# Performance work log

Hardware: AMD Instinct MI355X
Metric: run time of the kernel (lower is better)

Reference implementation:

```python
import jax, jax.numpy as jnp
import numpy as np
import math

L, B = 1024, 256
SEQ_DIM, KMER_DIM, HID = 16, 256, 64
N_LAYERS = 2
IN_DIM = SEQ_DIM + KMER_DIM + 21  # 293


def _normalize(v, eps=1e-12):
    return v / jnp.maximum(jnp.linalg.norm(v, axis=-1, keepdims=True), eps)


def _nerf_rot(a, b, c):
    # rotation matrix with columns [bc, n x bc, n] from last three backbone points
    bc = _normalize(c - b)
    n = _normalize(jnp.cross(b - a, bc))
    return jnp.stack([bc, jnp.cross(n, bc), n], axis=-1)  # (..., 3, 3)


def pnerf(c_tilde, nfrag):
    # c_tilde: (3L, B, 3) SRF coordinates; parallelized natural extension of reference frame
    Ltot, batch = c_tilde.shape[0], c_tilde.shape[1]
    k = Ltot // nfrag
    # contiguous fragments of length k, folded into the batch dim: (k, nfrag*B, 3)
    x = c_tilde.reshape(nfrag, k, batch, 3).transpose(1, 0, 2, 3).reshape(k, nfrag * batch, 3)
    init = jnp.array([[-math.sqrt(0.5), math.sqrt(1.5), 0.0],
                      [-math.sqrt(2.0), 0.0, 0.0],
                      [0.0, 0.0, 0.0]], dtype=c_tilde.dtype)
    F = nfrag * batch
    carry0 = (jnp.broadcast_to(init[0], (F, 3)),
              jnp.broadcast_to(init[1], (F, 3)),
              jnp.broadcast_to(init[2], (F, 3)))

    def extend(carry, ct):
        a, b, c = carry
        R = _nerf_rot(a, b, c)                      # (F, 3, 3)
        d = c + jnp.einsum('fij,fj->fi', R, ct)     # (F, 3)
        return (b, c, d), d

    _, frag = jax.lax.scan(extend, carry0, x)        # (k, F, 3)
    frag = frag.reshape(k, nfrag, batch, 3).transpose(1, 0, 2, 3)  # (nfrag, k, B, 3)

    # assemble fragments sequentially; init frame is identity/origin so frag 0 passes through
    carryA = (jnp.broadcast_to(init[0], (batch, 3)),
              jnp.broadcast_to(init[1], (batch, 3)),
              jnp.broadcast_to(init[2], (batch, 3)))

    def assemble(carry, fr):
        a, b, c = carry
        R = _nerf_rot(a, b, c)                      # (B, 3, 3)
        y = c + jnp.einsum('bij,kbj->kbi', R, fr)   # (k, B, 3)
        return (y[-3], y[-2], y[-1]), y

    _, ys = jax.lax.scan(assemble, carryA, frag)     # (nfrag, k, B, 3)
    return ys.reshape(nfrag * k, batch, 3)


def setup_inputs() -> dict:
    key = jax.random.key(0)
    ks = jax.random.split(key, 12)
    s = 0.05
    return {
        'seq': jax.random.randint(ks[0], (L, B), 0, 20, dtype=jnp.int64),
        'kmer': jax.random.randint(ks[1], (L, B), 0, 22 ** 3, dtype=jnp.int64),
        'pssm': jax.random.uniform(ks[2], (L, B, 21), dtype=jnp.float32),
        'length': jax.random.randint(ks[3], (L,), 1, L, dtype=jnp.int64),
        'seq_embed': jax.random.normal(ks[4], (20, SEQ_DIM), dtype=jnp.float32) * s,
        'kmer_embed': jax.random.normal(ks[5], (22 ** 3, KMER_DIM), dtype=jnp.float32) * s,
        'W0': jax.random.normal(ks[6], (IN_DIM, HID), dtype=jnp.float32) * s,
        'b0': jnp.zeros((HID,), dtype=jnp.float32),
        'We': jax.random.normal(ks[7], (HID, HID), dtype=jnp.float32) * s,
        'be': jnp.zeros((HID,), dtype=jnp.float32),
        'W1': jax.random.normal(ks[8], (HID, 9), dtype=jnp.float32) * s,
        'b1': jnp.zeros((9,), dtype=jnp.float32),
    }


def reference(seq, kmer, pssm, length, seq_embed, kmer_embed, W0, b0, We, be, W1, b1):
    s = seq_embed[seq]                                   # (L, B, 16)
    km = kmer_embed[kmer]                                # (L, B, 256)
    h = jnp.concatenate([s, km, pssm], axis=2)           # (L, B, 293)
    h = h @ W0 + b0                                      # (L, B, 64)
    # torch list-multiplication shares the SAME Linear across the n_layers blocks
    for _ in range(N_LAYERS):
        h = jax.nn.relu(h @ We + be)                     # dropout is identity at eval
    srf = h @ W1 + b1                                    # (L, B, 9)
    Ld, Bd = srf.shape[0], srf.shape[1]
    srf = srf.reshape(Ld, Bd, 3, 3).transpose(0, 2, 1, 3).reshape(3 * Ld, Bd, 3)
    return pnerf(srf, int(math.sqrt(Ld)))
```

## Files before the change

### kernel.cpp

```cpp
#include <hip/hip_runtime.h>
#include <math.h>

typedef short bf16x8 __attribute__((ext_vector_type(8)));
typedef float f32x4  __attribute__((ext_vector_type(4)));

__device__ __forceinline__ unsigned short f2bf(float x) {
    unsigned int u = __float_as_uint(x);
    return (unsigned short)((u + 0x7FFFu + ((u >> 16) & 1u)) >> 16);
}
__device__ __forceinline__ float bf2f(unsigned short h) {
    return __uint_as_float(((unsigned int)h) << 16);
}
__device__ __forceinline__ void split2(float x, unsigned short& h, unsigned short& l) {
    h = f2bf(x);
    l = f2bf(x - bf2f(h));
}
__device__ __forceinline__ void split2t(float x, unsigned short& h, unsigned short& l) {
    unsigned int u = __float_as_uint(x);
    h = (unsigned short)(u >> 16);
    float r = x - __uint_as_float(u & 0xFFFF0000u);
    l = f2bf(r);
}

__device__ __forceinline__ int hsw(int row, int col) {
    return (row << 6) + ((((col >> 3) ^ (row & 7)) << 3) | (col & 7));
}

__device__ __forceinline__ float inv_norm3(float x, float y, float z) {
    float d = fmaf(x, x, fmaf(y, y, z * z));
    return rsqrtf(fmaxf(d, 1e-24f));
}
__device__ __forceinline__ float3 f3sub(float3 a, float3 b) {
    return make_float3(a.x - b.x, a.y - b.y, a.z - b.z);
}
__device__ __forceinline__ float3 f3cross(float3 a, float3 b) {
    return make_float3(a.y * b.z - a.z * b.y,
                       a.z * b.x - a.x * b.z,
                       a.x * b.y - a.y * b.x);
}
__device__ __forceinline__ void nerf_frame(const float3& A, const float3& Bv,
                                           const float3& C, float3& bc,
                                           float3& n, float3& m3) {
    float3 w  = f3sub(C, Bv);
    float3 v  = f3sub(Bv, A);
    float3 cr = f3cross(v, w);
    float iw = inv_norm3(w.x, w.y, w.z);
    float ic = inv_norm3(cr.x, cr.y, cr.z);
    bc = make_float3(w.x * iw, w.y * iw, w.z * iw);
    n  = make_float3(cr.x * ic, cr.y * ic, cr.z * ic);
    m3 = f3cross(n, bc);
}
__device__ __forceinline__ float3 nerf_place(const float3& C, const float3& bc,
                                             const float3& m3, const float3& n,
                                             float tx, float ty, float tz) {
    return make_float3(
        fmaf(m3.x, ty, fmaf(bc.x, tx, fmaf(n.x, tz, C.x))),
        fmaf(m3.y, ty, fmaf(bc.y, tx, fmaf(n.y, tz, C.y))),
        fmaf(m3.z, ty, fmaf(bc.z, tx, fmaf(n.z, tz, C.z))));
}

struct KParams {
    const int* seq; const int* kmer; const float* pssm;
    const float* se; const float* emb;
    const float* W0; const float* b0; const float* We; const float* be;
    const float* W1; const float* b1;
    float* kmerT; float* seqT; float* srf_t; float* fragbuf;
    float4* frames; float* FPbuf; float* out;
    unsigned short *WeTH, *WeTL, *W0pTH, *W0pTL, *W1TH, *W1TL;
};

__global__ __launch_bounds__(256) void tables_kernel(KParams P) {
    const int tid = threadIdx.x;
    const int vb  = blockIdx.x;
    if (vb < 167) {
        const int lane = tid & 63;
        const int wv   = __builtin_amdgcn_readfirstlane(tid >> 6);
        const int q    = lane >> 4;
        const int c16  = lane & 15;
        const int r0   = vb * 64;
        const int n    = wv * 16 + c16;

        bf16x8 BH[8], BL[8];
        #pragma unroll
        for (int kt8 = 0; kt8 < 8; ++kt8)
            #pragma unroll
            for (int j = 0; j < 8; ++j) {
                float w = P.W0[(16 + kt8 * 32 + q * 8 + j) * 64 + n];
                unsigned short h, l; split2t(w, h, l);
                BH[kt8][j] = (short)h; BL[kt8][j] = (short)l;
            }
        f32x4 acc[4];
        #pragma unroll
        for (int t = 0; t < 4; ++t) acc[t] = (f32x4){0.f, 0.f, 0.f, 0.f};
        #pragma unroll
        for (int kt8 = 0; kt8 < 8; ++kt8) {
            #pragma unroll
            for (int t = 0; t < 4; ++t) {
                int rr = r0 + t * 16 + c16;
                if (rr > 10647) rr = 10647;
                const float* ap = P.emb + rr * 256 + kt8 * 32 + q * 8;
                float4 a0 = *(const float4*)ap;
                float4 a1 = *(const float4*)(ap + 4);
                bf16x8 ah, al;
                unsigned short h, l;
                split2t(a0.x, h, l); ah[0] = (short)h; al[0] = (short)l;
                split2t(a0.y, h, l); ah[1] = (short)h; al[1] = (short)l;
                split2t(a0.z, h, l); ah[2] = (short)h; al[2] = (short)l;
                split2t(a0.w, h, l); ah[3] = (short)h; al[3] = (short)l;
                split2t(a1.x, h, l); ah[4] = (short)h; al[4] = (short)l;
                split2t(a1.y, h, l); ah[5] = (short)h; al[5] = (short)l;
                split2t(a1.z, h, l); ah[6] = (short)h; al[6] = (short)l;
                split2t(a1.w, h, l); ah[7] = (short)h; al[7] = (short)l;
                acc[t] = __builtin_amdgcn_mfma_f32_16x16x32_bf16(ah, BH[kt8], acc[t], 0, 0, 0);
                acc[t] = __builtin_amdgcn_mfma_f32_16x16x32_bf16(al, BH[kt8], acc[t], 0, 0, 0);
                acc[t] = __builtin_amdgcn_mfma_f32_16x16x32_bf16(ah, BL[kt8], acc[t], 0, 0, 0);
            }
        }
        #pragma unroll
        for (int t = 0; t < 4; ++t)
            #pragma unroll
            for (int r = 0; r < 4; ++r) {
                int row = r0 + t * 16 + q * 4 + r;
                if (row < 10648) P.kmerT[row * 64 + n] = acc[t][r];
            }
    } else if (vb < 172) {
        int e = (vb - 167) * 256 + tid;
        int r = e >> 6, j = e & 63;
        float acc = P.b0[j];
        #pragma unroll
        for (int k = 0; k < 16; ++k)
            acc = fmaf(P.se[r * 16 + k], P.W0[k * 64 + j], acc);
        float cs = 0.f;
        #pragma unroll
        for (int c = 0; c < 21; ++c) cs += P.W0[(272 + c) * 64 + j];
        P.seqT[r * 64 + j] = acc + 0.5f * cs;
    } else {
        #pragma unroll
        for (int i = 0; i < 16; ++i) {
            int e = i * 256 + tid;
            int k = e >> 6, n = e & 63;
            unsigned short h, l; split2(P.We[k * 64 + n], h, l);
            P.WeTH[n * 64 + k] = h; P.WeTL[n * 64 + k] = l;
        }
        #pragma unroll
        for (int i = 0; i < 8; ++i) {
            int e = i * 256 + tid;
            int k = e >> 6, n = e & 63;
            float w = (k < 21) ? P.W0[(272 + k) * 64 + n] : 0.f;
            unsigned short h, l; split2(w, h, l);
            P.W0pTH[n * 32 + k] = h; P.W0pTL[n * 32 + k] = l;
        }
        #pragma unroll
        for (int i = 0; i < 4; ++i) {
            int e = i * 256 + tid;
            int k = e >> 4, c = e & 15;
            float w = (c < 9) ? P.W1[k * 9 + c] : 0.f;
            unsigned short h, l; split2(w, h, l);
            P.W1TH[c * 64 + k] = h; P.W1TL[c * 64 + k] = l;
        }
    }
}

__global__ __launch_bounds__(256, 4) void mlp_kernel(KParams P) {
    __shared__ __align__(16) unsigned char SMEM[32768];
    unsigned short* Hah = (unsigned short*)(SMEM);
    unsigned short* Hal = (unsigned short*)(SMEM + 8192);
    unsigned short* Hbh = (unsigned short*)(SMEM + 16384);
    unsigned short* Hbl = (unsigned short*)(SMEM + 24576);

    const int tid  = threadIdx.x;
    const int lane = tid & 63;
    const int wv   = __builtin_amdgcn_readfirstlane(tid >> 6);
    const int q    = lane >> 4;
    const int c16  = lane & 15;
    const int m0   = blockIdx.x * 64;
    const int n    = wv * 16 + c16;

    const int myseq = P.seq[m0 + lane];
    const int mykm  = P.kmer[m0 + lane];
    float g[4][4];
    #pragma unroll
    for (int t = 0; t < 4; ++t)
        #pragma unroll
        for (int r = 0; r < 4; ++r) {
            int src = (t * 16 + q * 4 + r) << 2;
            int s  = __builtin_amdgcn_ds_bpermute(src, myseq);
            int km = __builtin_amdgcn_ds_bpermute(src, mykm);
            g[t][r] = P.seqT[s * 64 + n] + P.kmerT[km * 64 + n];
        }

    bf16x8 pah[4], pal[4];
    #pragma unroll
    for (int t = 0; t < 4; ++t) {
        const float* prow = P.pssm + (m0 + t * 16 + c16) * 21;
        #pragma unroll
        for (int j = 0; j < 8; ++j) {
            const int col = q * 8 + j;
            float v = 0.f;
            if (col < 21) v = prow[col] - 0.5f;
            unsigned short h, l; split2t(v, h, l);
            pah[t][j] = (short)h; pal[t][j] = (short)l;
        }
    }

    bf16x8 WeH[2], WeL[2], W1H[2], W1L[2], W0H, W0L;
    #pragma unroll
    for (int kk = 0; kk < 2; ++kk) {
        WeH[kk] = *(const bf16x8*)(P.WeTH + n * 64 + kk * 32 + q * 8);
        WeL[kk] = *(const bf16x8*)(P.WeTL + n * 64 + kk * 32 + q * 8);
        W1H[kk] = *(const bf16x8*)(P.W1TH + c16 * 64 + kk * 32 + q * 8);
        W1L[kk] = *(const bf16x8*)(P.W1TL + c16 * 64 + kk * 32 + q * 8);
    }
    W0H = *(const bf16x8*)(P.W0pTH + n * 32 + q * 8);
    W0L = *(const bf16x8*)(P.W0pTL + n * 32 + q * 8);
    const float be_n = P.be[n];
    const float b1h  = (c16 < 9) ? P.b1[c16] : 0.f;

    f32x4 acc[4];
    #pragma unroll
    for (int t = 0; t < 4; ++t) acc[t] = (f32x4){0.f, 0.f, 0.f, 0.f};
    #pragma unroll
    for (int t = 0; t < 4; ++t) {
        acc[t] = __builtin_amdgcn_mfma_f32_16x16x32_bf16(pah[t], W0H, acc[t], 0, 0, 0);
        acc[t] = __builtin_amdgcn_mfma_f32_16x16x32_bf16(pal[t], W0H, acc[t], 0, 0, 0);
        acc[t] = __builtin_amdgcn_mfma_f32_16x16x32_bf16(pah[t], W0L, acc[t], 0, 0, 0);
    }
    #pragma unroll
    for (int t = 0; t < 4; ++t)
        #pragma unroll
        for (int r = 0; r < 4; ++r) {
            unsigned short h, l; split2t(acc[t][r] + g[t][r], h, l);
            Hah[hsw(t * 16 + q * 4 + r, n)] = h;
            Hal[hsw(t * 16 + q * 4 + r, n)] = l;
        }
    __syncthreads();

    {
        f32x4 a1[4];
        #pragma unroll
        for (int t = 0; t < 4; ++t) {
            a1[t] = (f32x4){be_n, be_n, be_n, be_n};
            #pragma unroll
            for (int kk = 0; kk < 2; ++kk) {
                bf16x8 ah = *(const bf16x8*)&Hah[hsw(t * 16 + c16, kk * 32 + q * 8)];
                bf16x8 al = *(const bf16x8*)&Hal[hsw(t * 16 + c16, kk * 32 + q * 8)];
                a1[t] = __builtin_amdgcn_mfma_f32_16x16x32_bf16(ah, WeH[kk], a1[t], 0, 0, 0);
                a1[t] = __builtin_amdgcn_mfma_f32_16x16x32_bf16(al, WeH[kk], a1[t], 0, 0, 0);
                a1[t] = __builtin_amdgcn_mfma_f32_16x16x32_bf16(ah, WeL[kk], a1[t], 0, 0, 0);
            }
        }
        #pragma unroll
        for (int t = 0; t < 4; ++t)
            #pragma unroll
            for (int r = 0; r < 4; ++r) {
                unsigned short h, l; split2t(fmaxf(a1[t][r], 0.f), h, l);
                Hbh[hsw(t * 16 + q * 4 + r, n)] = h;
                Hbl[hsw(t * 16 + q * 4 + r, n)] = l;
            }
        __syncthreads();
    }
    {
        f32x4 a2[4];
        #pragma unroll
        for (int t = 0; t < 4; ++t) {
            a2[t] = (f32x4){be_n, be_n, be_n, be_n};
            #pragma unroll
            for (int kk = 0; kk < 2; ++kk) {
                bf16x8 ah = *(const bf16x8*)&Hbh[hsw(t * 16 + c16, kk * 32 + q * 8)];
                bf16x8 al = *(const bf16x8*)&Hbl[hsw(t * 16 + c16, kk * 32 + q * 8)];
                a2[t] = __builtin_amdgcn_mfma_f32_16x16x32_bf16(ah, WeH[kk], a2[t], 0, 0, 0);
                a2[t] = __builtin_amdgcn_mfma_f32_16x16x32_bf16(al, WeH[kk], a2[t], 0, 0, 0);
                a2[t] = __builtin_amdgcn_mfma_f32_16x16x32_bf16(ah, WeL[kk], a2[t], 0, 0, 0);
            }
        }
        #pragma unroll
        for (int t = 0; t < 4; ++t)
            #pragma unroll
            for (int r = 0; r < 4; ++r) {
                unsigned short h, l; split2t(fmaxf(a2[t][r], 0.f), h, l);
                Hah[hsw(t * 16 + q * 4 + r, n)] = h;
                Hal[hsw(t * 16 + q * 4 + r, n)] = l;
            }
        __syncthreads();
    }
    {
        f32x4 ah4 = (f32x4){b1h, b1h, b1h, b1h};
        #pragma unroll
        for (int kk = 0; kk < 2; ++kk) {
            bf16x8 ah = *(const bf16x8*)&Hah[hsw(wv * 16 + c16, kk * 32 + q * 8)];
            bf16x8 al = *(const bf16x8*)&Hal[hsw(wv * 16 + c16, kk * 32 + q * 8)];
            ah4 = __builtin_amdgcn_mfma_f32_16x16x32_bf16(ah, W1H[kk], ah4, 0, 0, 0);
            ah4 = __builtin_amdgcn_mfma_f32_16x16x32_bf16(al, W1H[kk], ah4, 0, 0, 0);
            ah4 = __builtin_amdgcn_mfma_f32_16x16x32_bf16(ah, W1L[kk], ah4, 0, 0, 0);
        }
        if (c16 < 9) {
            #pragma unroll
            for (int r = 0; r < 4; ++r) {
                int pos = m0 + wv * 16 + q * 4 + r;
                int l = pos >> 8, b = pos & 255;
                P.srf_t[(l * 9 + c16) * 256 + b] = ah4[r];
            }
        }
    }
}

__global__ __launch_bounds__(64) void extend_kernel(KParams P) {
    int frag = blockIdx.x >> 2;
    int bb   = ((blockIdx.x & 3) << 6) + threadIdx.x;

    float3 A  = make_float3(-0.70710678118654752f, 1.22474487139158905f, 0.f);
    float3 Bv = make_float3(-1.41421356237309505f, 0.f, 0.f);
    float3 C  = make_float3(0.f, 0.f, 0.f);

    float ct0[9], ct1[9], ct2[9], ct3[9];
    #pragma unroll
    for (int m = 0; m < 9; ++m) {
        ct0[m] = P.srf_t[((frag * 32 + 0) * 9 + m) * 256 + bb];
        ct1[m] = P.srf_t[((frag * 32 + 1) * 9 + m) * 256 + bb];
        ct2[m] = P.srf_t[((frag * 32 + 2) * 9 + m) * 256 + bb];
    }
    for (int ll = 0; ll < 32; ++ll) {
        if (ll < 29) {
            #pragma unroll
            for (int m = 0; m < 9; ++m)
                ct3[m] = P.srf_t[((frag * 32 + ll + 3) * 9 + m) * 256 + bb];
        } else {
            #pragma unroll
            for (int m = 0; m < 9; ++m) ct3[m] = 0.f;
        }
        #pragma unroll
        for (int s3 = 0; s3 < 3; ++s3) {
            float3 bc, nn, m3;
            nerf_frame(A, Bv, C, bc, nn, m3);
            float3 d = nerf_place(C, bc, m3, nn,
                                  ct0[3 * s3 + 0], ct0[3 * s3 + 1], ct0[3 * s3 + 2]);
            int row = frag * 96 + ll * 3 + s3;
            P.fragbuf[(row * 3 + 0) * 256 + bb] = d.x;
            P.fragbuf[(row * 3 + 1) * 256 + bb] = d.y;
            P.fragbuf[(row * 3 + 2) * 256 + bb] = d.z;
            A = Bv; Bv = C; C = d;
        }
        #pragma unroll
        for (int m = 0; m < 9; ++m) { ct0[m] = ct1[m]; ct1[m] = ct2[m]; ct2[m] = ct3[m]; }
    }
    float3 bc, nn, m3;
    nerf_frame(A, Bv, C, bc, nn, m3);
    P.FPbuf[(frag * 12 + 0)  * 256 + bb] = bc.x;
    P.FPbuf[(frag * 12 + 1)  * 256 + bb] = bc.y;
    P.FPbuf[(frag * 12 + 2)  * 256 + bb] = bc.z;
    P.FPbuf[(frag * 12 + 3)  * 256 + bb] = m3.x;
    P.FPbuf[(frag * 12 + 4)  * 256 + bb] = m3.y;
    P.FPbuf[(frag * 12 + 5)  * 256 + bb] = m3.z;
    P.FPbuf[(frag * 12 + 6)  * 256 + bb] = nn.x;
    P.FPbuf[(frag * 12 + 7)  * 256 + bb] = nn.y;
    P.FPbuf[(frag * 12 + 8)  * 256 + bb] = nn.z;
    P.FPbuf[(frag * 12 + 9)  * 256 + bb] = C.x;
    P.FPbuf[(frag * 12 + 10) * 256 + bb] = C.y;
    P.FPbuf[(frag * 12 + 11) * 256 + bb] = C.z;
}

__global__ __launch_bounds__(256) void carry_kernel(KParams P) {
    __shared__ float S[384][16];
    const int tid  = threadIdx.x;
    const int base = blockIdx.x * 16;
    for (int i = tid; i < 384 * 16; i += 256) {
        int row = i >> 4, col = i & 15;
        S[row][col] = P.FPbuf[row * 256 + base + col];
    }
    __syncthreads();
    if (tid < 16) {
        int bb = base + tid;
        float3 ob = make_float3(1.f, 0.f, 0.f);
        float3 om = make_float3(0.f, 1.f, 0.f);
        float3 on = make_float3(0.f, 0.f, 1.f);
        float3 c  = make_float3(0.f, 0.f, 0.f);
        for (int f = 0; f < 32; ++f) {
            int fb = (f * 256 + bb) * 3;
            P.frames[fb + 0] = make_float4(ob.x, ob.y, ob.z, om.x);
            P.frames[fb + 1] = make_float4(om.y, om.z, on.x, on.y);
            P.frames[fb + 2] = make_float4(on.z, c.x, c.y, c.z);

            int r0 = f * 12;
            float3 Fb = make_float3(S[r0+0][tid], S[r0+1][tid], S[r0+2][tid]);
            float3 Fm = make_float3(S[r0+3][tid], S[r0+4][tid], S[r0+5][tid]);
            float3 Fn = make_float3(S[r0+6][tid], S[r0+7][tid], S[r0+8][tid]);
            float3 p  = make_float3(S[r0+9][tid], S[r0+10][tid], S[r0+11][tid]);

            float3 nb = make_float3(
                fmaf(ob.x,Fb.x, fmaf(om.x,Fb.y, on.x*Fb.z)),
                fmaf(ob.y,Fb.x, fmaf(om.y,Fb.y, on.y*Fb.z)),
                fmaf(ob.z,Fb.x, fmaf(om.z,Fb.y, on.z*Fb.z)));
            float3 nm = make_float3(
                fmaf(ob.x,Fm.x, fmaf(om.x,Fm.y, on.x*Fm.z)),
                fmaf(ob.y,Fm.x, fmaf(om.y,Fm.y, on.y*Fm.z)),
                fmaf(ob.z,Fm.x, fmaf(om.z,Fm.y, on.z*Fm.z)));
            float3 nn2 = make_float3(
                fmaf(ob.x,Fn.x, fmaf(om.x,Fn.y, on.x*Fn.z)),
                fmaf(ob.y,Fn.x, fmaf(om.y,Fn.y, on.y*Fn.z)),
                fmaf(ob.z,Fn.x, fmaf(om.z,Fn.y, on.z*Fn.z)));
            float3 nc = make_float3(
                fmaf(ob.x,p.x, fmaf(om.x,p.y, fmaf(on.x,p.z, c.x))),
                fmaf(ob.y,p.x, fmaf(om.y,p.y, fmaf(on.y,p.z, c.y))),
                fmaf(ob.z,p.x, fmaf(om.z,p.y, fmaf(on.z,p.z, c.z))));
            ob = nb; om = nm; on = nn2; c = nc;
        }
    }
}

__global__ __launch_bounds__(256) void apply_kernel(KParams P) {
    __shared__ float sm[768];
    const int bb = threadIdx.x;
    #pragma unroll 1
    for (int i = 0; i < 4; ++i) {
        const int row  = blockIdx.x * 4 + i;
        const int frag = row / 96;

        float fx = P.fragbuf[(row * 3 + 0) * 256 + bb];
        float fy = P.fragbuf[(row * 3 + 1) * 256 + bb];
        float fz = P.fragbuf[(row * 3 + 2) * 256 + bb];

        int fb = (frag * 256 + bb) * 3;
        float4 f0 = P.frames[fb + 0];
        float4 f1 = P.frames[fb + 1];
        float4 f2 = P.frames[fb + 2];

        float ox = f2.y + f0.x * fx + f0.w * fy + f1.z * fz;
        float oy = f2.z + f0.y * fx + f1.x * fy + f1.w * fz;
        float oz = f2.w + f0.z * fx + f1.y * fy + f2.x * fz;

        __syncthreads();
        sm[bb * 3 + 0] = ox;
        sm[bb * 3 + 1] = oy;
        sm[bb * 3 + 2] = oz;
        __syncthreads();

        int base = row * 768;
        P.out[base + bb]       = sm[bb];
        P.out[base + 256 + bb] = sm[256 + bb];
        P.out[base + 512 + bb] = sm[512 + bb];
    }
}

extern "C" void kernel_launch(void* const* d_in, const int* in_sizes, int n_in,
                              void* d_out, int out_size, void* d_ws, size_t ws_size,
                              hipStream_t stream) {
    float* ws      = (float*)d_ws;
    float* kmerT   = ws;
    float* seqT    = kmerT + 681472;
    float* srf_t   = seqT + 1280;
    float* fragbuf = srf_t + 2359296;
    float* frames  = fragbuf + 2359296;
    float* FPbuf   = frames + 98304;

    unsigned short* WeTH  = (unsigned short*)fragbuf;
    unsigned short* WeTL  = WeTH + 4096;
    unsigned short* W0pTH = WeTL + 4096;
    unsigned short* W0pTL = W0pTH + 2048;
    unsigned short* W1TH  = W0pTL + 2048;
    unsigned short* W1TL  = W1TH + 1024;

    KParams P;
    P.seq  = (const int*)d_in[0];
    P.kmer = (const int*)d_in[1];
    P.pssm = (const float*)d_in[2];
    P.se   = (const float*)d_in[4];
    P.emb  = (const float*)d_in[5];
    P.W0   = (const float*)d_in[6];
    P.b0   = (const float*)d_in[7];
    P.We   = (const float*)d_in[8];
    P.be   = (const float*)d_in[9];
    P.W1   = (const float*)d_in[10];
    P.b1   = (const float*)d_in[11];
    P.kmerT = kmerT; P.seqT = seqT; P.srf_t = srf_t; P.fragbuf = fragbuf;
    P.frames = (float4*)frames; P.FPbuf = FPbuf; P.out = (float*)d_out;
    P.WeTH = WeTH; P.WeTL = WeTL; P.W0pTH = W0pTH; P.W0pTL = W0pTL;
    P.W1TH = W1TH; P.W1TL = W1TL;

    hipLaunchKernelGGL(tables_kernel, dim3(173),  dim3(256), 0, stream, P);
    hipLaunchKernelGGL(mlp_kernel,    dim3(4096), dim3(256), 0, stream, P);
    hipLaunchKernelGGL(extend_kernel, dim3(128),  dim3(64),  0, stream, P);
    hipLaunchKernelGGL(carry_kernel,  dim3(16),   dim3(256), 0, stream, P);
    hipLaunchKernelGGL(apply_kernel,  dim3(768),  dim3(256), 0, stream, P);
}
```

Measured before the change: 197.7 us.

## Shrink MLP block to 16 rows, stage PSSM via LDS, raise occupancy

Each MLP block now handles 16 rows instead of 64, so the grid grows fourfold and LDS per block drops from 32KB to 8KB. Launch bounds are raised to allow 8 blocks per CU. The PSSM tile is loaded cooperatively into LDS once, and the final W1 projection runs only in wave 0. This cuts registers and LDS per block to increase occupancy and latency hiding, at the cost of more blocks, reloading the weight fragments per block, and idle waves during the last stage.

```diff
diff --git a/kernel.cpp b/kernel.cpp
--- a/kernel.cpp
+++ b/kernel.cpp
@@ -161,134 +161,130 @@
     }
 }
 
-__global__ __launch_bounds__(256, 4) void mlp_kernel(KParams P) {
-    __shared__ __align__(16) unsigned char SMEM[32768];
+__global__ __launch_bounds__(256, 8) void mlp_kernel(KParams P) {
+    __shared__ __align__(16) unsigned char SMEM[8192];
     unsigned short* Hah = (unsigned short*)(SMEM);
-    unsigned short* Hal = (unsigned short*)(SMEM + 8192);
-    unsigned short* Hbh = (unsigned short*)(SMEM + 16384);
-    unsigned short* Hbl = (unsigned short*)(SMEM + 24576);
+    unsigned short* Hal = (unsigned short*)(SMEM + 2048);
+    unsigned short* Hbh = (unsigned short*)(SMEM + 4096);
+    unsigned short* Hbl = (unsigned short*)(SMEM + 6144);
+    unsigned short (*Pph)[40] = (unsigned short (*)[40])(SMEM + 4096);
+    unsigned short (*Ppl)[40] = (unsigned short (*)[40])(SMEM + 4096 + 1280);
 
     const int tid  = threadIdx.x;
     const int lane = tid & 63;
     const int wv   = __builtin_amdgcn_readfirstlane(tid >> 6);
     const int q    = lane >> 4;
     const int c16  = lane & 15;
-    const int m0   = blockIdx.x * 64;
+    const int m0   = blockIdx.x * 16;
     const int n    = wv * 16 + c16;
 
-    const int myseq = P.seq[m0 + lane];
-    const int mykm  = P.kmer[m0 + lane];
-    float g[4][4];
+    int sidx[4], kidx[4];
     #pragma unroll
-    for (int t = 0; t < 4; ++t)
-        #pragma unroll
-        for (int r = 0; r < 4; ++r) {
-            int src = (t * 16 + q * 4 + r) << 2;
-            int s  = __builtin_amdgcn_ds_bpermute(src, myseq);
-            int km = __builtin_amdgcn_ds_bpermute(src, mykm);
-            g[t][r] = P.seqT[s * 64 + n] + P.kmerT[km * 64 + n];
-        }
-
-    bf16x8 pah[4], pal[4];
+    for (int r = 0; r < 4; ++r) {
+        sidx[r] = P.seq[m0 + q * 4 + r];
+        kidx[r] = P.kmer[m0 + q * 4 + r];
+    }
+    float g[4];
     #pragma unroll
-    for (int t = 0; t < 4; ++t) {
-        const float* prow = P.pssm + (m0 + t * 16 + c16) * 21;
-        #pragma unroll
-        for (int j = 0; j < 8; ++j) {
-            const int col = q * 8 + j;
-            float v = 0.f;
-            if (col < 21) v = prow[col] - 0.5f;
-            unsigned short h, l; split2t(v, h, l);
-            pah[t][j] = (short)h; pal[t][j] = (short)l;
-        }
-    }
-
-    bf16x8 WeH[2], WeL[2], W1H[2], W1L[2], W0H, W0L;
+    for (int r = 0; r < 4; ++r)
+        g[r] = P.seqT[sidx[r] * 64 + n] + P.kmerT[kidx[r] * 64 + n];
+
+    {
+        const int row_s = tid >> 4;
+        const int c_s   = tid & 15;
+        const float* pr = P.pssm + (m0 + row_s) * 21;
+        unsigned short h, l;
+        float v = pr[c_s] - 0.5f;
+        split2t(v, h, l);
+        Pph[row_s][c_s] = h; Ppl[row_s][c_s] = l;
+        if (c_s < 5) {
+            float v2 = pr[16 + c_s] - 0.5f;
+            split2t(v2, h, l);
+            Pph[row_s][16 + c_s] = h; Ppl[row_s][16 + c_s] = l;
+        }
+        if (c_s < 11) {
+            Pph[row_s][21 + c_s] = 0; Ppl[row_s][21 + c_s] = 0;
+        }
+    }
+
+    bf16x8 WeH[2], WeL[2], W0H, W0L;
     #pragma unroll
     for (int kk = 0; kk < 2; ++kk) {
         WeH[kk] = *(const bf16x8*)(P.WeTH + n * 64 + kk * 32 + q * 8);
         WeL[kk] = *(const bf16x8*)(P.WeTL + n * 64 + kk * 32 + q * 8);
-        W1H[kk] = *(const bf16x8*)(P.W1TH + c16 * 64 + kk * 32 + q * 8);
-        W1L[kk] = *(const bf16x8*)(P.W1TL + c16 * 64 + kk * 32 + q * 8);
     }
     W0H = *(const bf16x8*)(P.W0pTH + n * 32 + q * 8);
     W0L = *(const bf16x8*)(P.W0pTL + n * 32 + q * 8);
     const float be_n = P.be[n];
-    const float b1h  = (c16 < 9) ? P.b1[c16] : 0.f;
-
-    f32x4 acc[4];
-    #pragma unroll
-    for (int t = 0; t < 4; ++t) acc[t] = (f32x4){0.f, 0.f, 0.f, 0.f};
-    #pragma unroll
-    for (int t = 0; t < 4; ++t) {
-        acc[t] = __builtin_amdgcn_mfma_f32_16x16x32_bf16(pah[t], W0H, acc[t], 0, 0, 0);
-        acc[t] = __builtin_amdgcn_mfma_f32_16x16x32_bf16(pal[t], W0H, acc[t], 0, 0, 0);
-        acc[t] = __builtin_amdgcn_mfma_f32_16x16x32_bf16(pah[t], W0L, acc[t], 0, 0, 0);
-    }
-    #pragma unroll
-    for (int t = 0; t < 4; ++t)
+    __syncthreads();
+
+    {
+        bf16x8 pah = *(const bf16x8*)&Pph[c16][q * 8];
+        bf16x8 pal = *(const bf16x8*)&Ppl[c16][q * 8];
+        f32x4 a0 = (f32x4){0.f, 0.f, 0.f, 0.f};
+        a0 = __builtin_amdgcn_mfma_f32_16x16x32_bf16(pah, W0H, a0, 0, 0, 0);
+        a0 = __builtin_amdgcn_mfma_f32_16x16x32_bf16(pal, W0H, a0, 0, 0, 0);
+        a0 = __builtin_amdgcn_mfma_f32_16x16x32_bf16(pah, W0L, a0, 0, 0, 0);
         #pragma unroll
         for (int r = 0; r < 4; ++r) {
-            unsigned short h, l; split2t(acc[t][r] + g[t][r], h, l);
-            Hah[hsw(t * 16 + q * 4 + r, n)] = h;
-            Hal[hsw(t * 16 + q * 4 + r, n)] = l;
-        }
+            unsigned short h, l; split2t(a0[r] + g[r], h, l);
+            Hah[hsw(q * 4 + r, n)] = h;
+            Hal[hsw(q * 4 + r, n)] = l;
+        }
+    }
     __syncthreads();
 
     {
-        f32x4 a1[4];
-        #pragma unroll
-        for (int t = 0; t < 4; ++t) {
-            a1[t] = (f32x4){be_n, be_n, be_n, be_n};
-            #pragma unroll
-            for (int kk = 0; kk < 2; ++kk) {
-                bf16x8 ah = *(const bf16x8*)&Hah[hsw(t * 16 + c16, kk * 32 + q * 8)];
-                bf16x8 al = *(const bf16x8*)&Hal[hsw(t * 16 + c16, kk * 32 + q * 8)];
-                a1[t] = __builtin_amdgcn_mfma_f32_16x16x32_bf16(ah, WeH[kk], a1[t], 0, 0, 0);
-                a1[t] = __builtin_amdgcn_mfma_f32_16x16x32_bf16(al, WeH[kk], a1[t], 0, 0, 0);
-                a1[t] = __builtin_amdgcn_mfma_f32_16x16x32_bf16(ah, WeL[kk], a1[t], 0, 0, 0);
-            }
-        }
-        #pragma unroll
-        for (int t = 0; t < 4; ++t)
-            #pragma unroll
-            for (int r = 0; r < 4; ++r) {
-                unsigned short h, l; split2t(fmaxf(a1[t][r], 0.f), h, l);
-                Hbh[hsw(t * 16 + q * 4 + r, n)] = h;
-                Hbl[hsw(t * 16 + q * 4 + r, n)] = l;
-            }
-        __syncthreads();
-    }
+        f32x4 a1 = (f32x4){be_n, be_n, be_n, be_n};
+        #pragma unroll
+        for (int kk = 0; kk < 2; ++kk) {
+            bf16x8 ah = *(const bf16x8*)&Hah[hsw(c16, kk * 32 + q * 8)];
+            bf16x8 al = *(const bf16x8*)&Hal[hsw(c16, kk * 32 + q * 8)];
+            a1 = __builtin_amdgcn_mfma_f32_16x16x32_bf16(ah, WeH[kk], a1, 0, 0, 0);
+            a1 = __builtin_amdgcn_mfma_f32_16x16x32_bf16(al, WeH[kk], a1, 0, 0, 0);
+            a1 = __builtin_amdgcn_mfma_f32_16x16x32_bf16(ah, WeL[kk], a1, 0, 0, 0);
+        }
+        #pragma unroll
+        for (int r = 0; r < 4; ++r) {
+            unsigned short h, l; split2t(fmaxf(a1[r], 0.f), h, l);
+            Hbh[hsw(q * 4 + r, n)] = h;
+            Hbl[hsw(q * 4 + r, n)] = l;
+        }
+    }
+    __syncthreads();
+
     {
-        f32x4 a2[4];
-        #pragma unroll
-        for (int t = 0; t < 4; ++t) {
-            a2[t] = (f32x4){be_n, be_n, be_n, be_n};
-            #pragma unroll
-            for (int kk = 0; kk < 2; ++kk) {
-                bf16x8 ah = *(const bf16x8*)&Hbh[hsw(t * 16 + c16, kk * 32 + q * 8)];
-                bf16x8 al = *(const bf16x8*)&Hbl[hsw(t * 16 + c16, kk * 32 + q * 8)];
-                a2[t] = __builtin_amdgcn_mfma_f32_16x16x32_bf16(ah, WeH[kk], a2[t], 0, 0, 0);
-                a2[t] = __builtin_amdgcn_mfma_f32_16x16x32_bf16(al, WeH[kk], a2[t], 0, 0, 0);
-                a2[t] = __builtin_amdgcn_mfma_f32_16x16x32_bf16(ah, WeL[kk], a2[t], 0, 0, 0);
-            }
-        }
-        #pragma unroll
-        for (int t = 0; t < 4; ++t)
-            #pragma unroll
-            for (int r = 0; r < 4; ++r) {
-                unsigned short h, l; split2t(fmaxf(a2[t][r], 0.f), h, l);
-                Hah[hsw(t * 16 + q * 4 + r, n)] = h;
-                Hal[hsw(t * 16 + q * 4 + r, n)] = l;
-            }
-        __syncthreads();
-    }
-    {
+        f32x4 a2 = (f32x4){be_n, be_n, be_n, be_n};
+        #pragma unroll
+        for (int kk = 0; kk < 2; ++kk) {
+            bf16x8 ah = *(const bf16x8*)&Hbh[hsw(c16, kk * 32 + q * 8)];
+            bf16x8 al = *(const bf16x8*)&Hbl[hsw(c16, kk * 32 + q * 8)];
+            a2 = __builtin_amdgcn_mfma_f32_16x16x32_bf16(ah, WeH[kk], a2, 0, 0, 0);
+            a2 = __builtin_amdgcn_mfma_f32_16x16x32_bf16(al, WeH[kk], a2, 0, 0, 0);
+            a2 = __builtin_amdgcn_mfma_f32_16x16x32_bf16(ah, WeL[kk], a2, 0, 0, 0);
+        }
+        #pragma unroll
+        for (int r = 0; r < 4; ++r) {
+            unsigned short h, l; split2t(fmaxf(a2[r], 0.f), h, l);
+            Hah[hsw(q * 4 + r, n)] = h;
+            Hal[hsw(q * 4 + r, n)] = l;
+        }
+    }
+    __syncthreads();
+
+    if (wv == 0) {
+        bf16x8 W1H[2], W1L[2];
+        #pragma unroll
+        for (int kk = 0; kk < 2; ++kk) {
+            W1H[kk] = *(const bf16x8*)(P.W1TH + c16 * 64 + kk * 32 + q * 8);
+            W1L[kk] = *(const bf16x8*)(P.W1TL + c16 * 64 + kk * 32 + q * 8);
+        }
+        const float b1h = (c16 < 9) ? P.b1[c16] : 0.f;
         f32x4 ah4 = (f32x4){b1h, b1h, b1h, b1h};
         #pragma unroll
         for (int kk = 0; kk < 2; ++kk) {
-            bf16x8 ah = *(const bf16x8*)&Hah[hsw(wv * 16 + c16, kk * 32 + q * 8)];
-            bf16x8 al = *(const bf16x8*)&Hal[hsw(wv * 16 + c16, kk * 32 + q * 8)];
+            bf16x8 ah = *(const bf16x8*)&Hah[hsw(c16, kk * 32 + q * 8)];
+            bf16x8 al = *(const bf16x8*)&Hal[hsw(c16, kk * 32 + q * 8)];
             ah4 = __builtin_amdgcn_mfma_f32_16x16x32_bf16(ah, W1H[kk], ah4, 0, 0, 0);
             ah4 = __builtin_amdgcn_mfma_f32_16x16x32_bf16(al, W1H[kk], ah4, 0, 0, 0);
             ah4 = __builtin_amdgcn_mfma_f32_16x16x32_bf16(ah, W1L[kk], ah4, 0, 0, 0);
@@ -296,7 +292,7 @@
         if (c16 < 9) {
             #pragma unroll
             for (int r = 0; r < 4; ++r) {
-                int pos = m0 + wv * 16 + q * 4 + r;
+                int pos = m0 + q * 4 + r;
                 int l = pos >> 8, b = pos & 255;
                 P.srf_t[(l * 9 + c16) * 256 + b] = ah4[r];
             }
@@ -476,9 +472,9 @@
     P.WeTH = WeTH; P.WeTL = WeTL; P.W0pTH = W0pTH; P.W0pTL = W0pTL;
     P.W1TH = W1TH; P.W1TL = W1TL;
 
-    hipLaunchKernelGGL(tables_kernel, dim3(173),  dim3(256), 0, stream, P);
-    hipLaunchKernelGGL(mlp_kernel,    dim3(4096), dim3(256), 0, stream, P);
-    hipLaunchKernelGGL(extend_kernel, dim3(128),  dim3(64),  0, stream, P);
-    hipLaunchKernelGGL(carry_kernel,  dim3(16),   dim3(256), 0, stream, P);
-    hipLaunchKernelGGL(apply_kernel,  dim3(768),  dim3(256), 0, stream, P);
-}
+    hipLaunchKernelGGL(tables_kernel, dim3(173),   dim3(256), 0, stream, P);
+    hipLaunchKernelGGL(mlp_kernel,    dim3(16384), dim3(256), 0, stream, P);
+    hipLaunchKernelGGL(extend_kernel, dim3(128),   dim3(64),  0, stream, P);
+    hipLaunchKernelGGL(carry_kernel,  dim3(16),    dim3(256), 0, stream, P);
+    hipLaunchKernelGGL(apply_kernel,  dim3(768),   dim3(256), 0, stream, P);
+}
```

Result: faster. 192.1 us (-2.8%).
